# Performance work log

Hardware: AMD Instinct MI355X
Metric: run time of the kernel (lower is better)

Reference implementation:

```python
import jax, jax.numpy as jnp
import numpy as np

NUM_CODES = 4096
CODE_DIM = 256
COMMITMENT_COST = 0.25
DIVERSITY_WEIGHT = 0.1
B = 65536


def setup_inputs() -> dict:
    key = jax.random.key(0)
    kz, ke = jax.random.split(key)
    z = jax.random.normal(kz, (B, CODE_DIM), dtype=jnp.float32)
    embedding = jax.random.normal(ke, (NUM_CODES, CODE_DIM), dtype=jnp.float32)
    return {"z": z, "embedding": embedding}


def reference(z, embedding):
    # distances [B, K] = ||z||^2 + ||e||^2 - 2 z e^T
    distances = (
        jnp.sum(z * z, axis=1, keepdims=True)
        + jnp.sum(embedding * embedding, axis=1)
        - 2.0 * z @ embedding.T
    )
    indices = jnp.argmin(distances, axis=1)  # [B] int
    z_q = embedding[indices]                  # [B, D]

    sg = jax.lax.stop_gradient
    commitment_loss = jnp.mean((z - sg(z_q)) ** 2)
    embedding_loss = jnp.mean((sg(z) - z_q) ** 2)

    # diversity regularizer over soft assignments
    soft = jax.nn.softmax(-distances, axis=1)        # [B, K]
    avg_soft = jnp.mean(soft, axis=0)                # [K]
    entropy = -jnp.sum(avg_soft * jnp.log(avg_soft + 1e-10))
    max_entropy = jnp.log(jnp.float32(NUM_CODES))
    diversity_loss = max_entropy - entropy

    vq_loss = (
        commitment_loss * COMMITMENT_COST
        + embedding_loss
        + DIVERSITY_WEIGHT * diversity_loss
    )

    # straight-through estimator
    z_q_st = z + sg(z_q - z)

    # perplexity from hard assignments (bincount == one-hot mean)
    avg_probs = jnp.bincount(indices, length=NUM_CODES).astype(jnp.float32) / B
    perplexity = jnp.exp(-jnp.sum(avg_probs * jnp.log(avg_probs + 1e-10)))

    return (z_q_st, vq_loss, perplexity, indices, diversity_loss)
```

## Files before the change

kernel.cpp:

```cpp
#include <hip/hip_runtime.h>
#include <cstdint>
#include <cstddef>


#define NROWS     65536
#define NCODES    4096
#define DDIM      256
#define CAND_CAP  24
#define UMARGIN   1.0f
#define USKIP     8.5f

typedef _Float16 half8 __attribute__((ext_vector_type(8)));
typedef _Float16 half4 __attribute__((ext_vector_type(4)));
typedef float    f32x4 __attribute__((ext_vector_type(4)));

#define WS_BINCNT   0u
#define WS_ZERO_END 16384u
#define WS_CANDCNT  16384u
#define WS_SPART    278528u
#define WS_EF16     8667136u
#define WS_EE       10764288u
#define WS_ROWD     10780672u
#define WS_CANDIDX  11042816u
#define WS_TE       17334272u
#define WS_TP       17367040u
#define WS_END      17399808u

__device__ __forceinline__ void gload_lds16(const void* g, void* lds) {
    __builtin_amdgcn_global_load_lds(
        (const __attribute__((address_space(1))) unsigned int*)g,
        (__attribute__((address_space(3))) unsigned int*)lds, 16, 0, 0);
}

__global__ __launch_bounds__(256)
void prep_kernel(const float* __restrict__ src, _Float16* __restrict__ dst,
                 float* __restrict__ norms)
{
    const int tid = threadIdx.x;
    const int w = tid >> 6, l = tid & 63;
    const int row = blockIdx.x * 4 + w;
    const float4 v = *(const float4*)(src + (size_t)row * DDIM + l * 4);
    half4 h;
    h[0] = (_Float16)v.x; h[1] = (_Float16)v.y;
    h[2] = (_Float16)v.z; h[3] = (_Float16)v.w;
    *(half4*)(dst + (size_t)row * DDIM + l * 4) = h;
    double s = (double)v.x * v.x + (double)v.y * v.y
             + (double)v.z * v.z + (double)v.w * v.w;
#pragma unroll
    for (int off = 1; off < 64; off <<= 1) s += __shfl_xor(s, off, 64);
    if (l == 0) norms[row] = (float)s;
}

__global__ __launch_bounds__(256, 2)
void sweep_fused_kernel(const float* __restrict__ z, const _Float16* __restrict__ ef,
                        const float* __restrict__ ee, float* __restrict__ Spart,
                        int* __restrict__ cand_cnt, int* __restrict__ cand_idx)
{
    __shared__ _Float16 Bl[2][64 * 256];
    __shared__ float Sl[NCODES];

    const int tid = threadIdx.x;
    const int w = tid >> 6, l = tid & 63;
    const int lg = l >> 4, lc = l & 15;
    const int row0 = blockIdx.x * 128;

    half8 af[2][8];
#pragma unroll
    for (int fr = 0; fr < 2; ++fr)
#pragma unroll
    for (int ksl = 0; ksl < 8; ++ksl) {
        const float* zp = z + (size_t)(row0 + w * 32 + fr * 16 + lc) * DDIM + ksl * 32 + lg * 8;
        const float4 v0 = *(const float4*)zp;
        const float4 v1 = *(const float4*)(zp + 4);
        half8 h;
        h[0] = (_Float16)v0.x; h[1] = (_Float16)v0.y; h[2] = (_Float16)v0.z; h[3] = (_Float16)v0.w;
        h[4] = (_Float16)v1.x; h[5] = (_Float16)v1.y; h[6] = (_Float16)v1.z; h[7] = (_Float16)v1.w;
        af[fr][ksl] = h;
    }

    for (int i = tid; i < NCODES; i += 256) Sl[i] = 0.0f;

    int soff[8];
#pragma unroll
    for (int it = 0; it < 8; ++it) {
        const int it_g = w * 8 + it;
        const int ksl = it_g >> 2, cf = it_g & 3;
        soff[it] = (cf * 16 + lc) * 512 + ksl * 64 + lg * 16;
    }
    const char* efb = (const char*)ef;
    char* blb = (char*)&Bl[0][0];

    float pmx[8], pZ[8];
#pragma unroll
    for (int i = 0; i < 8; ++i) { pmx[i] = -1e30f; pZ[i] = 0.0f; }
    int bcnt[8];
#pragma unroll
    for (int i = 0; i < 8; ++i) bcnt[i] = 0;

    float eevc[4];
#pragma unroll
    for (int cf = 0; cf < 4; ++cf) eevc[cf] = ee[cf * 16 + lc];
#pragma unroll
    for (int it = 0; it < 8; ++it)
        gload_lds16(efb + soff[it], blb + (w * 8 + it) * 1024);
    __syncthreads();

    for (int s = 0; s < 128; ++s) {
        const int cur = s & 1;
        const int nt = s & 63;
        const int nnt = (s + 1) & 63;

        float eevn[4];
#pragma unroll
        for (int cf = 0; cf < 4; ++cf) eevn[cf] = ee[nnt * 64 + cf * 16 + lc];

        if (s < 127) {
            const char* src = efb + ((size_t)nnt << 15);
            char* dst = blb + (cur ^ 1) * 32768;
#pragma unroll
            for (int it = 0; it < 8; ++it)
                gload_lds16(src + soff[it], dst + (w * 8 + it) * 1024);
        }

        f32x4 acc[2][4];
#pragma unroll
        for (int cf = 0; cf < 4; ++cf) {
            const float eh = -0.5f * eevc[cf];
            acc[0][cf] = (f32x4){eh, eh, eh, eh};
            acc[1][cf] = (f32x4){eh, eh, eh, eh};
        }

        const char* bb = blb + cur * 32768 + (l << 4);
#pragma unroll
        for (int ksl = 0; ksl < 8; ++ksl) {
#pragma unroll
            for (int cf = 0; cf < 4; ++cf) {
                const half8 b = *(const half8*)(bb + (ksl * 4 + cf) * 1024);
                acc[0][cf] = __builtin_amdgcn_mfma_f32_16x16x32_f16(af[0][ksl], b, acc[0][cf], 0, 0, 0);
                acc[1][cf] = __builtin_amdgcn_mfma_f32_16x16x32_f16(af[1][ksl], b, acc[1][cf], 0, 0, 0);
            }
        }

        if (s < 64) {
#pragma unroll
            for (int fr = 0; fr < 2; ++fr)
#pragma unroll
            for (int reg = 0; reg < 4; ++reg) {
                const int ri = fr * 4 + reg;
                const float u0 = acc[fr][0][reg];
                const float u1 = acc[fr][1][reg];
                const float u2 = acc[fr][2][reg];
                const float u3 = acc[fr][3][reg];
                const float mloc = fmaxf(fmaxf(u0, u1), fmaxf(u2, u3));
                float m = pmx[ri];
                if (mloc > m - USKIP) {
                    if (mloc > m) { pZ[ri] *= __expf(2.0f * (m - mloc)); m = mloc; pmx[ri] = m; }
                    pZ[ri] += __expf(2.0f * (u0 - m)) + __expf(2.0f * (u1 - m))
                            + __expf(2.0f * (u2 - m)) + __expf(2.0f * (u3 - m));
                }
            }
        } else {
            float sp[4] = {0.f, 0.f, 0.f, 0.f};
#pragma unroll
            for (int fr = 0; fr < 2; ++fr)
#pragma unroll
            for (int reg = 0; reg < 4; ++reg) {
                const int ri = fr * 4 + reg;
                const float m = pmx[ri], iz = pZ[ri];
                const float u0 = acc[fr][0][reg];
                const float u1 = acc[fr][1][reg];
                const float u2 = acc[fr][2][reg];
                const float u3 = acc[fr][3][reg];
#pragma unroll
                for (int cf = 0; cf < 4; ++cf) {
                    const float u = acc[fr][cf][reg];
                    const bool hit = (u >= m - UMARGIN);
                    const unsigned long long mk = __ballot(hit);
                    if (mk) {
                        const unsigned grp = (unsigned)((mk >> (lg * 16)) & 0xFFFFull);
                        const int slot = bcnt[ri] + __popc(grp & ((1u << lc) - 1u));
                        if (hit && slot < CAND_CAP) {
                            const int rg_ = row0 + w * 32 + fr * 16 + lg * 4 + reg;
                            cand_idx[(size_t)rg_ * CAND_CAP + slot] = nt * 64 + cf * 16 + lc;
                        }
                        bcnt[ri] += __popc(grp);
                    }
                }
                const float umax = fmaxf(fmaxf(u0, u1), fmaxf(u2, u3));
                if (umax >= m - USKIP) {
                    sp[0] += __expf(2.0f * (u0 - m)) * iz;
                    sp[1] += __expf(2.0f * (u1 - m)) * iz;
                    sp[2] += __expf(2.0f * (u2 - m)) * iz;
                    sp[3] += __expf(2.0f * (u3 - m)) * iz;
                }
            }
#pragma unroll
            for (int cf = 0; cf < 4; ++cf) {
                float v = sp[cf];
                v += __shfl_xor(v, 16, 64);
                v += __shfl_xor(v, 32, 64);
                if (l < 16) atomicAdd(&Sl[nt * 64 + cf * 16 + l], v);
            }
        }

        if (s == 63) {
#pragma unroll
            for (int ri = 0; ri < 8; ++ri) {
                float m = pmx[ri], Zv = pZ[ri];
#pragma unroll
                for (int off = 1; off < 16; off <<= 1) {
                    const float mo = __shfl_xor(m, off, 64);
                    const float Zo = __shfl_xor(Zv, off, 64);
                    const float mn = fmaxf(m, mo);
                    Zv = Zv * __expf(2.0f * (m - mn)) + Zo * __expf(2.0f * (mo - mn));
                    m = mn;
                }
                pmx[ri] = m;
                pZ[ri] = 1.0f / Zv;
            }
        }

        __syncthreads();
#pragma unroll
        for (int cf = 0; cf < 4; ++cf) eevc[cf] = eevn[cf];
    }

    if (lc == 0) {
#pragma unroll
        for (int fr = 0; fr < 2; ++fr)
#pragma unroll
        for (int reg = 0; reg < 4; ++reg)
            cand_cnt[row0 + w * 32 + fr * 16 + lg * 4 + reg] = bcnt[fr * 4 + reg];
    }

    for (int i = tid; i < NCODES; i += 256)
        Spart[(size_t)blockIdx.x * NCODES + i] = Sl[i];
}

__global__ __launch_bounds__(256)
void refine_kernel(const float* __restrict__ z, const float* __restrict__ emb,
                   const int* __restrict__ cand_cnt, const int* __restrict__ cand_idx,
                   float* __restrict__ out_zq, float* __restrict__ out_idx,
                   unsigned int* __restrict__ bincnt, float* __restrict__ rowD)
{
    const int tid = threadIdx.x;
    const int w = tid >> 6, l = tid & 63;
    const int row = blockIdx.x * 4 + w;
    const float4 zv = *(const float4*)(z + (size_t)row * DDIM + l * 4);
    const double z0 = zv.x, z1 = zv.y, z2 = zv.z, z3 = zv.w;
    const int craw = cand_cnt[row];
    const int cnt = craw < 1 ? 1 : (craw > CAND_CAP ? CAND_CAP : craw);
    double dmin = 1e300; int kmin = 0;
    for (int c = 0; c < cnt; ++c) {
        int k = (craw < 1) ? 0 : cand_idx[(size_t)row * CAND_CAP + c];
        k &= (NCODES - 1);
        const float4 ev = *(const float4*)(emb + (size_t)k * DDIM + l * 4);
        const double t0 = z0 - ev.x, t1 = z1 - ev.y, t2 = z2 - ev.z, t3 = z3 - ev.w;
        double s = t0 * t0 + t1 * t1 + t2 * t2 + t3 * t3;
#pragma unroll
        for (int off = 1; off < 64; off <<= 1) s += __shfl_xor(s, off, 64);
        if (s < dmin || (s == dmin && k < kmin)) { dmin = s; kmin = k; }
    }
    const float4 bv = *(const float4*)(emb + (size_t)kmin * DDIM + l * 4);
    *(float4*)(out_zq + (size_t)row * DDIM + l * 4) = bv;
    if (l == 0) {
        out_idx[row] = (float)kmin;
        atomicAdd(&bincnt[kmin], 1u);
        rowD[row] = (float)dmin;
    }
}

__global__ __launch_bounds__(256)
void reduce1_kernel(const float* __restrict__ Spart, const unsigned int* __restrict__ bincnt,
                    const float* __restrict__ rowD,
                    double* __restrict__ te, double* __restrict__ tp, double* __restrict__ tm)
{
    const int k = blockIdx.x * 256 + threadIdx.x;
    double s = 0.0;
#pragma unroll 8
    for (int wg = 0; wg < 512; ++wg) s += (double)Spart[(size_t)wg * NCODES + k];
    const double avg = s * (1.0 / 65536.0);
    te[k] = avg * log(avg + 1e-10);
    const double ap = (double)bincnt[k] * (1.0 / 65536.0);
    tp[k] = ap * log(ap + 1e-10);
    double dm = 0.0;
#pragma unroll
    for (int j = 0; j < 16; ++j) dm += (double)rowD[k * 16 + j];
    tm[k] = dm;
}

__global__ __launch_bounds__(256)
void reduce2_kernel(const double* __restrict__ te, const double* __restrict__ tp,
                    const double* __restrict__ tm, float* __restrict__ out)
{
    __shared__ double sa[256], sb[256], sc[256];
    const int tid = threadIdx.x;
    double a = 0.0, b = 0.0, c = 0.0;
    for (int i = tid; i < NCODES; i += 256) { a += te[i]; b += tp[i]; c += tm[i]; }
    sa[tid] = a; sb[tid] = b; sc[tid] = c;
    __syncthreads();
    for (int s = 128; s > 0; s >>= 1) {
        if (tid < s) { sa[tid] += sa[tid + s]; sb[tid] += sb[tid + s]; sc[tid] += sc[tid + s]; }
        __syncthreads();
    }
    if (tid == 0) {
        const double entropy    = -sa[0];
        const double diversity  = log(4096.0) - entropy;
        const double perplexity = exp(-sb[0]);
        const double mse        = sc[0] * (1.0 / 16777216.0);
        const double vq         = 1.25 * mse + 0.1 * diversity;
        out[16777216] = (float)vq;
        out[16777217] = (float)perplexity;
        out[16842754] = (float)diversity;
    }
}

extern "C" void kernel_launch(void* const* d_in, const int* in_sizes, int n_in,
                              void* d_out, int out_size, void* d_ws, size_t ws_size,
                              hipStream_t stream)
{
    const float* z   = (const float*)d_in[0];
    const float* emb = (const float*)d_in[1];
    float* out = (float*)d_out;
    char* ws = (char*)d_ws;
    if (ws_size < (size_t)WS_END) return;

    unsigned int* bincnt   = (unsigned int*)(ws + WS_BINCNT);
    int*          cand_cnt = (int*)(ws + WS_CANDCNT);
    float*        Spart    = (float*)(ws + WS_SPART);
    _Float16*     ef16     = (_Float16*)(ws + WS_EF16);
    float*        ee       = (float*)(ws + WS_EE);
    float*        rowD     = (float*)(ws + WS_ROWD);
    int*          cand_idx = (int*)(ws + WS_CANDIDX);
    double*       te       = (double*)(ws + WS_TE);
    double*       tp       = (double*)(ws + WS_TP);
    double*       tm       = (double*)(ws + WS_CANDIDX);

    hipMemsetAsync(d_ws, 0, WS_ZERO_END, stream);
    hipLaunchKernelGGL(prep_kernel, dim3(NCODES / 4), dim3(256), 0, stream, emb, ef16, ee);
    hipLaunchKernelGGL(sweep_fused_kernel, dim3(NROWS / 128), dim3(256), 0, stream,
                       z, ef16, ee, Spart, cand_cnt, cand_idx);
    hipLaunchKernelGGL(refine_kernel, dim3(NROWS / 4), dim3(256), 0, stream,
                       z, emb, cand_cnt, cand_idx, out, out + 16777218, bincnt, rowD);
    hipLaunchKernelGGL(reduce1_kernel, dim3(16), dim3(256), 0, stream, Spart, bincnt, rowD, te, tp, tm);
    hipLaunchKernelGGL(reduce2_kernel, dim3(1), dim3(256), 0, stream, te, tp, tm, out);
}
```

Baseline: 427.5 us.

## Software-pipeline sweep loop so epilogue of previous tile overlaps MFMAs

Double-buffers the MFMA accumulators so each sweep step issues the matrix multiplies for tile s while running the softmax/candidate epilogue on tile s-1's results. The loop is manually unrolled by two to alternate accumulator sets, with a final epilogue after the loop. This aims to hide the exp/ballot/atomic epilogue latency behind MFMA execution, at the cost of 32 extra accumulator registers, which risks spills or lower occupancy under launch_bounds(256,2).

```diff
diff --git a/kernel.cpp b/kernel.cpp
--- a/kernel.cpp
+++ b/kernel.cpp
@@ -51,6 +51,152 @@
     if (l == 0) norms[row] = (float)s;
 }
 
+__device__ __forceinline__ void epi_phase0(const f32x4 (&acc)[2][4],
+                                           float (&pmx)[8], float (&pZ)[8])
+{
+#pragma unroll
+    for (int fr = 0; fr < 2; ++fr)
+#pragma unroll
+    for (int reg = 0; reg < 4; ++reg) {
+        const int ri = fr * 4 + reg;
+        const float u0 = acc[fr][0][reg];
+        const float u1 = acc[fr][1][reg];
+        const float u2 = acc[fr][2][reg];
+        const float u3 = acc[fr][3][reg];
+        const float mloc = fmaxf(fmaxf(u0, u1), fmaxf(u2, u3));
+        float m = pmx[ri];
+        if (mloc > m - USKIP) {
+            if (mloc > m) { pZ[ri] *= __expf(2.0f * (m - mloc)); m = mloc; pmx[ri] = m; }
+            pZ[ri] += __expf(2.0f * (u0 - m)) + __expf(2.0f * (u1 - m))
+                    + __expf(2.0f * (u2 - m)) + __expf(2.0f * (u3 - m));
+        }
+    }
+}
+
+__device__ __forceinline__ void epi_merge(float (&pmx)[8], float (&pZ)[8])
+{
+#pragma unroll
+    for (int ri = 0; ri < 8; ++ri) {
+        float m = pmx[ri], Zv = pZ[ri];
+#pragma unroll
+        for (int off = 1; off < 16; off <<= 1) {
+            const float mo = __shfl_xor(m, off, 64);
+            const float Zo = __shfl_xor(Zv, off, 64);
+            const float mn = fmaxf(m, mo);
+            Zv = Zv * __expf(2.0f * (m - mn)) + Zo * __expf(2.0f * (mo - mn));
+            m = mn;
+        }
+        pmx[ri] = m;
+        pZ[ri] = 1.0f / Zv;
+    }
+}
+
+__device__ __forceinline__ void epi_phase1(const f32x4 (&acc)[2][4],
+                                           const float (&pmx)[8], const float (&pZ)[8],
+                                           int (&bcnt)[8], float* __restrict__ Sl,
+                                           int* __restrict__ cand_idx, const int nt,
+                                           const int row0, const int w,
+                                           const int lg, const int lc, const int l)
+{
+    float sp[4] = {0.f, 0.f, 0.f, 0.f};
+#pragma unroll
+    for (int fr = 0; fr < 2; ++fr)
+#pragma unroll
+    for (int reg = 0; reg < 4; ++reg) {
+        const int ri = fr * 4 + reg;
+        const float m = pmx[ri], iz = pZ[ri];
+        const float u0 = acc[fr][0][reg];
+        const float u1 = acc[fr][1][reg];
+        const float u2 = acc[fr][2][reg];
+        const float u3 = acc[fr][3][reg];
+#pragma unroll
+        for (int cf = 0; cf < 4; ++cf) {
+            const float u = acc[fr][cf][reg];
+            const bool hit = (u >= m - UMARGIN);
+            const unsigned long long mk = __ballot(hit);
+            if (mk) {
+                const unsigned grp = (unsigned)((mk >> (lg * 16)) & 0xFFFFull);
+                const int slot = bcnt[ri] + __popc(grp & ((1u << lc) - 1u));
+                if (hit && slot < CAND_CAP) {
+                    const int rg_ = row0 + w * 32 + fr * 16 + lg * 4 + reg;
+                    cand_idx[(size_t)rg_ * CAND_CAP + slot] = nt * 64 + cf * 16 + lc;
+                }
+                bcnt[ri] += __popc(grp);
+            }
+        }
+        const float umax = fmaxf(fmaxf(u0, u1), fmaxf(u2, u3));
+        if (umax >= m - USKIP) {
+            sp[0] += __expf(2.0f * (u0 - m)) * iz;
+            sp[1] += __expf(2.0f * (u1 - m)) * iz;
+            sp[2] += __expf(2.0f * (u2 - m)) * iz;
+            sp[3] += __expf(2.0f * (u3 - m)) * iz;
+        }
+    }
+#pragma unroll
+    for (int cf = 0; cf < 4; ++cf) {
+        float v = sp[cf];
+        v += __shfl_xor(v, 16, 64);
+        v += __shfl_xor(v, 32, 64);
+        if (l < 16) atomicAdd(&Sl[nt * 64 + cf * 16 + l], v);
+    }
+}
+
+__device__ __forceinline__ void sweep_step(
+    const int s, f32x4 (&accC)[2][4], f32x4 (&accP)[2][4],
+    float (&eevc)[4], float (&eevn)[4],
+    const half8 (&af)[2][8], char* __restrict__ blb, const char* __restrict__ efb,
+    const float* __restrict__ ee, const int (&soff)[8],
+    float (&pmx)[8], float (&pZ)[8], int (&bcnt)[8],
+    float* __restrict__ Sl, int* __restrict__ cand_idx,
+    const int row0, const int w, const int l, const int lg, const int lc)
+{
+    const int cur = s & 1;
+    const int nnt = (s + 1) & 63;
+
+#pragma unroll
+    for (int cf = 0; cf < 4; ++cf) eevn[cf] = ee[nnt * 64 + cf * 16 + lc];
+
+    if (s < 127) {
+        const char* src = efb + ((size_t)nnt << 15);
+        char* dst = blb + (cur ^ 1) * 32768;
+#pragma unroll
+        for (int it = 0; it < 8; ++it)
+            gload_lds16(src + soff[it], dst + (w * 8 + it) * 1024);
+    }
+
+#pragma unroll
+    for (int cf = 0; cf < 4; ++cf) {
+        const float eh = -0.5f * eevc[cf];
+        accC[0][cf] = (f32x4){eh, eh, eh, eh};
+        accC[1][cf] = (f32x4){eh, eh, eh, eh};
+    }
+
+    const char* bb = blb + cur * 32768 + (l << 4);
+#pragma unroll
+    for (int ksl = 0; ksl < 8; ++ksl) {
+#pragma unroll
+        for (int cf = 0; cf < 4; ++cf) {
+            const half8 b = *(const half8*)(bb + (ksl * 4 + cf) * 1024);
+            accC[0][cf] = __builtin_amdgcn_mfma_f32_16x16x32_f16(af[0][ksl], b, accC[0][cf], 0, 0, 0);
+            accC[1][cf] = __builtin_amdgcn_mfma_f32_16x16x32_f16(af[1][ksl], b, accC[1][cf], 0, 0, 0);
+        }
+    }
+
+    if (s >= 1) {
+        const int sprev = s - 1;
+        if (sprev < 64) {
+            epi_phase0(accP, pmx, pZ);
+            if (sprev == 63) epi_merge(pmx, pZ);
+        } else {
+            epi_phase1(accP, pmx, pZ, bcnt, Sl, cand_idx, sprev & 63, row0, w, lg, lc, l);
+        }
+    }
+
+    __syncthreads();
+#pragma unroll
+    for (int cf = 0; cf < 4; ++cf) eevc[cf] = eevn[cf];
+}
+
 __global__ __launch_bounds__(256, 2)
 void sweep_fused_kernel(const float* __restrict__ z, const _Float16* __restrict__ ef,
                         const float* __restrict__ ee, float* __restrict__ Spart,
@@ -97,7 +243,7 @@
 #pragma unroll
     for (int i = 0; i < 8; ++i) bcnt[i] = 0;
 
-    float eevc[4];
+    float eevc[4], eevn[4];
 #pragma unroll
     for (int cf = 0; cf < 4; ++cf) eevc[cf] = ee[cf * 16 + lc];
 #pragma unroll
@@ -105,125 +251,20 @@
         gload_lds16(efb + soff[it], blb + (w * 8 + it) * 1024);
     __syncthreads();
 
-    for (int s = 0; s < 128; ++s) {
-        const int cur = s & 1;
-        const int nt = s & 63;
-        const int nnt = (s + 1) & 63;
-
-        float eevn[4];
-#pragma unroll
-        for (int cf = 0; cf < 4; ++cf) eevn[cf] = ee[nnt * 64 + cf * 16 + lc];
-
-        if (s < 127) {
-            const char* src = efb + ((size_t)nnt << 15);
-            char* dst = blb + (cur ^ 1) * 32768;
-#pragma unroll
-            for (int it = 0; it < 8; ++it)
-                gload_lds16(src + soff[it], dst + (w * 8 + it) * 1024);
-        }
-
-        f32x4 acc[2][4];
-#pragma unroll
-        for (int cf = 0; cf < 4; ++cf) {
-            const float eh = -0.5f * eevc[cf];
-            acc[0][cf] = (f32x4){eh, eh, eh, eh};
-            acc[1][cf] = (f32x4){eh, eh, eh, eh};
-        }
-
-        const char* bb = blb + cur * 32768 + (l << 4);
-#pragma unroll
-        for (int ksl = 0; ksl < 8; ++ksl) {
-#pragma unroll
-            for (int cf = 0; cf < 4; ++cf) {
-                const half8 b = *(const half8*)(bb + (ksl * 4 + cf) * 1024);
-                acc[0][cf] = __builtin_amdgcn_mfma_f32_16x16x32_f16(af[0][ksl], b, acc[0][cf], 0, 0, 0);
-                acc[1][cf] = __builtin_amdgcn_mfma_f32_16x16x32_f16(af[1][ksl], b, acc[1][cf], 0, 0, 0);
-            }
-        }
-
-        if (s < 64) {
-#pragma unroll
-            for (int fr = 0; fr < 2; ++fr)
-#pragma unroll
-            for (int reg = 0; reg < 4; ++reg) {
-                const int ri = fr * 4 + reg;
-                const float u0 = acc[fr][0][reg];
-                const float u1 = acc[fr][1][reg];
-                const float u2 = acc[fr][2][reg];
-                const float u3 = acc[fr][3][reg];
-                const float mloc = fmaxf(fmaxf(u0, u1), fmaxf(u2, u3));
-                float m = pmx[ri];
-                if (mloc > m - USKIP) {
-                    if (mloc > m) { pZ[ri] *= __expf(2.0f * (m - mloc)); m = mloc; pmx[ri] = m; }
-                    pZ[ri] += __expf(2.0f * (u0 - m)) + __expf(2.0f * (u1 - m))
-                            + __expf(2.0f * (u2 - m)) + __expf(2.0f * (u3 - m));
-                }
-            }
-        } else {
-            float sp[4] = {0.f, 0.f, 0.f, 0.f};
-#pragma unroll
-            for (int fr = 0; fr < 2; ++fr)
-#pragma unroll
-            for (int reg = 0; reg < 4; ++reg) {
-                const int ri = fr * 4 + reg;
-                const float m = pmx[ri], iz = pZ[ri];
-                const float u0 = acc[fr][0][reg];
-                const float u1 = acc[fr][1][reg];
-                const float u2 = acc[fr][2][reg];
-                const float u3 = acc[fr][3][reg];
-#pragma unroll
-                for (int cf = 0; cf < 4; ++cf) {
-                    const float u = acc[fr][cf][reg];
-                    const bool hit = (u >= m - UMARGIN);
-                    const unsigned long long mk = __ballot(hit);
-                    if (mk) {
-                        const unsigned grp = (unsigned)((mk >> (lg * 16)) & 0xFFFFull);
-                        const int slot = bcnt[ri] + __popc(grp & ((1u << lc) - 1u));
-                        if (hit && slot < CAND_CAP) {
-                            const int rg_ = row0 + w * 32 + fr * 16 + lg * 4 + reg;
-                            cand_idx[(size_t)rg_ * CAND_CAP + slot] = nt * 64 + cf * 16 + lc;
-                        }
-                        bcnt[ri] += __popc(grp);
-                    }
-                }
-                const float umax = fmaxf(fmaxf(u0, u1), fmaxf(u2, u3));
-                if (umax >= m - USKIP) {
-                    sp[0] += __expf(2.0f * (u0 - m)) * iz;
-                    sp[1] += __expf(2.0f * (u1 - m)) * iz;
-                    sp[2] += __expf(2.0f * (u2 - m)) * iz;
-                    sp[3] += __expf(2.0f * (u3 - m)) * iz;
-                }
-            }
-#pragma unroll
-            for (int cf = 0; cf < 4; ++cf) {
-                float v = sp[cf];
-                v += __shfl_xor(v, 16, 64);
-                v += __shfl_xor(v, 32, 64);
-                if (l < 16) atomicAdd(&Sl[nt * 64 + cf * 16 + l], v);
-            }
-        }
-
-        if (s == 63) {
-#pragma unroll
-            for (int ri = 0; ri < 8; ++ri) {
-                float m = pmx[ri], Zv = pZ[ri];
-#pragma unroll
-                for (int off = 1; off < 16; off <<= 1) {
-                    const float mo = __shfl_xor(m, off, 64);
-                    const float Zo = __shfl_xor(Zv, off, 64);
-                    const float mn = fmaxf(m, mo);
-                    Zv = Zv * __expf(2.0f * (m - mn)) + Zo * __expf(2.0f * (mo - mn));
-                    m = mn;
-                }
-                pmx[ri] = m;
-                pZ[ri] = 1.0f / Zv;
-            }
-        }
-
-        __syncthreads();
-#pragma unroll
-        for (int cf = 0; cf < 4; ++cf) eevc[cf] = eevn[cf];
-    }
+    f32x4 accA[2][4], accB[2][4];
+
+    sweep_step(0, accA, accB, eevc, eevn, af, blb, efb, ee, soff,
+               pmx, pZ, bcnt, Sl, cand_idx, row0, w, l, lg, lc);
+    for (int sp = 0; sp < 63; ++sp) {
+        sweep_step(2 * sp + 1, accB, accA, eevc, eevn, af, blb, efb, ee, soff,
+                   pmx, pZ, bcnt, Sl, cand_idx, row0, w, l, lg, lc);
+        sweep_step(2 * sp + 2, accA, accB, eevc, eevn, af, blb, efb, ee, soff,
+                   pmx, pZ, bcnt, Sl, cand_idx, row0, w, l, lg, lc);
+    }
+    sweep_step(127, accB, accA, eevc, eevn, af, blb, efb, ee, soff,
+               pmx, pZ, bcnt, Sl, cand_idx, row0, w, l, lg, lc);
+    epi_phase1(accB, pmx, pZ, bcnt, Sl, cand_idx, 63, row0, w, lg, lc, l);
+    __syncthreads();
 
     if (lc == 0) {
 #pragma unroll
```

New measurement: 466.3 us. +9.1%, slower.
